# Kernel tuning notes

Hardware: AMD Instinct MI355X
Metric: run time of the kernel (lower is better)

Reference implementation:

```python
import jax, jax.numpy as jnp
import numpy as np

N = 100_000      # target ('paper') nodes
E_RAND = 500_000 # random metapath edges (self-loops added on top)
C = 256          # channels
H = 8            # heads
D = C // H       # proj_dim = 32
SEM = 128        # semantic attention hidden
NEG_SLOPE = 0.2


def _edges(k):
    e = jax.random.randint(k, (2, E_RAND), 0, N, dtype=jnp.int32)
    loops = jnp.broadcast_to(jnp.arange(N, dtype=jnp.int32), (2, N))
    return jnp.concatenate([e, loops], axis=1)  # [2, E_RAND + N]


def setup_inputs() -> dict:
    key = jax.random.key(0)
    ks = jax.random.split(key, 9)
    return {
        "x": jax.random.normal(ks[0], (N, C), dtype=jnp.float32),
        "W": jax.random.normal(ks[1], (D, C), dtype=jnp.float32) * (1.0 / np.sqrt(C)),
        "att1": jax.random.normal(ks[2], (H, 2 * D), dtype=jnp.float32) * (1.0 / np.sqrt(2 * D)),
        "att2": jax.random.normal(ks[3], (H, 2 * D), dtype=jnp.float32) * (1.0 / np.sqrt(2 * D)),
        "fc_w": jax.random.normal(ks[4], (SEM, C), dtype=jnp.float32) * (1.0 / np.sqrt(C)),
        "fc_b": jnp.zeros((SEM,), dtype=jnp.float32),
        "q": jax.random.normal(ks[5], (SEM,), dtype=jnp.float32) * (1.0 / np.sqrt(SEM)),
        "ei1": _edges(ks[6]),
        "ei2": _edges(ks[7]),
    }


def _segment_softmax(e, dst, num_nodes):
    # numerically stable softmax over edges grouped by destination node
    m = jax.ops.segment_max(e, dst, num_segments=num_nodes)      # [N, H]
    ex = jnp.exp(e - m[dst])                                     # [E, H]
    s = jax.ops.segment_sum(ex, dst, num_segments=num_nodes)     # [N, H]
    return ex / s[dst]


def _gat_layer(h, ei, att):
    # h: [N, d] projected target features; ei: [2, E]; att: [H, 2d]
    src, dst = ei[0], ei[1]
    n, d = h.shape
    a_dst, a_src = att[:, :d], att[:, d:]   # cat order in torch: [h_i(dst), h_j(src)]
    # per-edge attention logits [E, H] without materializing [E, H, 2d]
    e = jax.nn.leaky_relu(h[dst] @ a_dst.T + h[src] @ a_src.T, NEG_SLOPE)
    alpha = _segment_softmax(e, dst, n)                          # [E, H]
    m = h[src][:, None, :] * alpha[:, :, None]                   # [E, H, d]
    out = jax.ops.segment_sum(m, dst, num_segments=n)            # [N, H, d]
    return jax.nn.elu(out).reshape(n, H * d)                     # [N, H*d]


def reference(x, W, att1, att2, fc_w, fc_b, q, ei1, ei2):
    # type-specific projection (bias-free Linear): [N, C] -> [N, d]
    h = x @ W.T
    Z1 = _gat_layer(h, ei1, att1)
    Z2 = _gat_layer(h, ei2, att2)
    # semantic attention across meta-paths
    def score(Z):
        return (jnp.tanh(Z @ fc_w.T + fc_b) @ q).mean()
    V = jax.nn.softmax(jnp.stack([score(Z1), score(Z2)]))        # [2]
    return V[0] * Z1 + V[1] * Z2                                 # [N, C]
```

## Files before the change

kernel.cpp:

```cpp
#include <hip/hip_runtime.h>
#include <math.h>

#define Nn 100000
#define Cc 256
#define Dd 32
#define Hh 8
#define SEMk 128
#define PAD 32
#define NEG 0.2f

typedef __attribute__((ext_vector_type(8))) short bf16x8;
typedef __attribute__((ext_vector_type(4))) short s16x4;
typedef __attribute__((ext_vector_type(4))) float f32x4;

__device__ __forceinline__ short f2bf(float f) {
    unsigned u = __float_as_uint(f);
    u = (u + 0x7FFF + ((u >> 16) & 1)) >> 16;
    return (short)u;
}

__global__ __launch_bounds__(256) void k_wtrans(const float* __restrict__ W,
                                                float* __restrict__ Wt) {
    int i = blockIdx.x * 256 + threadIdx.x;
    if (i < Dd * Cc) {
        int j = i >> 5, k = i & 31;
        Wt[i] = W[k * Cc + j];
    }
}

__global__ __launch_bounds__(256) void k_fcwb(const float* __restrict__ fcw,
                                              short* __restrict__ fcwb) {
    int i = blockIdx.x * 256 + threadIdx.x;
    if (i < SEMk * Cc) fcwb[i] = f2bf(fcw[i]);
}

__global__ __launch_bounds__(256) void k_hproj(const float* __restrict__ x,
                                               const float* __restrict__ Wt,
                                               const float* __restrict__ att1,
                                               const float* __restrict__ att2,
                                               float* __restrict__ h,
                                               float* __restrict__ sd1, float* __restrict__ ss1,
                                               float* __restrict__ sd2, float* __restrict__ ss2) {
    __shared__ float4 xs[32 * 65];
    __shared__ float  wt[256 * 36];
    __shared__ float4 hs[32 * 9];
    __shared__ float  a1[8 * 68];
    __shared__ float  a2[8 * 68];

    int t = threadIdx.x;
    int nb = blockIdx.x * 32;

    const float4* xg = (const float4*)x + (size_t)nb * 64;
#pragma unroll
    for (int it = 0; it < 8; ++it) {
        int i = t + it * 256;
        xs[(i >> 6) * 65 + (i & 63)] = xg[i];
    }
    const float4* wg = (const float4*)Wt;
#pragma unroll
    for (int it = 0; it < 8; ++it) {
        int i = t + it * 256;
        *(float4*)&wt[(i >> 3) * 36 + (i & 7) * 4] = wg[i];
    }
#pragma unroll
    for (int it = 0; it < 2; ++it) {
        int i = t + it * 256;
        a1[(i >> 6) * 68 + (i & 63)] = att1[i];
        a2[(i >> 6) * 68 + (i & 63)] = att2[i];
    }
    __syncthreads();

    int nl = t >> 3;
    int dq = t & 7;
    float4 acc = make_float4(0.f, 0.f, 0.f, 0.f);
    const float4* xr = &xs[nl * 65];
#pragma unroll 4
    for (int j4 = 0; j4 < 64; ++j4) {
        float4 xv = xr[j4];
        float4 w0 = *(const float4*)&wt[(j4 * 4 + 0) * 36 + dq * 4];
        float4 w1 = *(const float4*)&wt[(j4 * 4 + 1) * 36 + dq * 4];
        float4 w2 = *(const float4*)&wt[(j4 * 4 + 2) * 36 + dq * 4];
        float4 w3 = *(const float4*)&wt[(j4 * 4 + 3) * 36 + dq * 4];
        acc.x += xv.x * w0.x + xv.y * w1.x + xv.z * w2.x + xv.w * w3.x;
        acc.y += xv.x * w0.y + xv.y * w1.y + xv.z * w2.y + xv.w * w3.y;
        acc.z += xv.x * w0.z + xv.y * w1.z + xv.z * w2.z + xv.w * w3.z;
        acc.w += xv.x * w0.w + xv.y * w1.w + xv.z * w2.w + xv.w * w3.w;
    }
    ((float4*)h)[(size_t)(nb + nl) * 8 + dq] = acc;
    hs[nl * 9 + dq] = acc;
    __syncthreads();

    int nl2 = t >> 3;
    int hh = t & 7;
    float d1 = 0.f, s1 = 0.f, d2 = 0.f, s2 = 0.f;
#pragma unroll
    for (int d4 = 0; d4 < 8; ++d4) {
        float4 hv = hs[nl2 * 9 + d4];
        float4 ad1 = *(const float4*)&a1[hh * 68 + d4 * 4];
        float4 as1 = *(const float4*)&a1[hh * 68 + 32 + d4 * 4];
        float4 ad2 = *(const float4*)&a2[hh * 68 + d4 * 4];
        float4 as2 = *(const float4*)&a2[hh * 68 + 32 + d4 * 4];
        d1 += hv.x * ad1.x + hv.y * ad1.y + hv.z * ad1.z + hv.w * ad1.w;
        s1 += hv.x * as1.x + hv.y * as1.y + hv.z * as1.z + hv.w * as1.w;
        d2 += hv.x * ad2.x + hv.y * ad2.y + hv.z * ad2.z + hv.w * ad2.w;
        s2 += hv.x * as2.x + hv.y * as2.y + hv.z * as2.z + hv.w * as2.w;
    }
    int n = nb + nl2;
    sd1[n * 8 + hh] = d1; ss1[n * 8 + hh] = s1;
    sd2[n * 8 + hh] = d2; ss2[n * 8 + hh] = s2;
}

__global__ __launch_bounds__(256) void k_scatter(const int* __restrict__ ei, int E,
                                                 int* __restrict__ cnt, int* __restrict__ slots) {
    int e = blockIdx.x * 256 + threadIdx.x;
    if (e >= E) return;
    int s = ei[e];
    int d = ei[E + e];
    int pos = atomicAdd(&cnt[d], 1);
    if (pos < PAD) slots[d * PAD + pos] = s;
}

__global__ __launch_bounds__(256) void k_gat(const float* __restrict__ h,
                                             const float* __restrict__ sdst,
                                             const float* __restrict__ ssrc,
                                             const int* __restrict__ cnt,
                                             const int* __restrict__ slots,
                                             float* __restrict__ Z) {
    int gid = blockIdx.x * 256 + threadIdx.x;
    int n = gid >> 6;
    int lane = gid & 63;
    if (n >= Nn) return;
    int deg = cnt[n]; if (deg > PAD) deg = PAD;
    int hh = lane >> 3;
    int sub = lane & 7;
    float sd = sdst[n * 8 + hh];
    int sval = slots[n * PAD + (lane & 31)];
    const float4* h4 = (const float4*)h;

    float ssum = 0.f;
    float4 acc = make_float4(0.f, 0.f, 0.f, 0.f);

    int cs0 = __shfl(sval, 0);
    int cs1 = __shfl(sval, 1);
    int cs2 = __shfl(sval, 2);
    int cs3 = __shfl(sval, 3);
    cs1 = (1 < deg) ? cs1 : n;
    cs2 = (2 < deg) ? cs2 : n;
    cs3 = (3 < deg) ? cs3 : n;
    float  ca0 = ssrc[(size_t)cs0 * 8 + hh];
    float  ca1 = ssrc[(size_t)cs1 * 8 + hh];
    float  ca2 = ssrc[(size_t)cs2 * 8 + hh];
    float  ca3 = ssrc[(size_t)cs3 * 8 + hh];
    float4 cv0 = h4[(size_t)cs0 * 8 + sub];
    float4 cv1 = h4[(size_t)cs1 * 8 + sub];
    float4 cv2 = h4[(size_t)cs2 * 8 + sub];
    float4 cv3 = h4[(size_t)cs3 * 8 + sub];

    int base = 0;
    for (;;) {
        int nb = base + 4;
        bool more = nb < deg;
        int ns0, ns1, ns2, ns3;
        float na0, na1, na2, na3;
        float4 nv0, nv1, nv2, nv3;
        if (more) {
            ns0 = __shfl(sval, nb + 0);
            ns1 = __shfl(sval, nb + 1);
            ns2 = __shfl(sval, nb + 2);
            ns3 = __shfl(sval, nb + 3);
            ns1 = (nb + 1 < deg) ? ns1 : n;
            ns2 = (nb + 2 < deg) ? ns2 : n;
            ns3 = (nb + 3 < deg) ? ns3 : n;
            na0 = ssrc[(size_t)ns0 * 8 + hh];
            na1 = ssrc[(size_t)ns1 * 8 + hh];
            na2 = ssrc[(size_t)ns2 * 8 + hh];
            na3 = ssrc[(size_t)ns3 * 8 + hh];
            nv0 = h4[(size_t)ns0 * 8 + sub];
            nv1 = h4[(size_t)ns1 * 8 + sub];
            nv2 = h4[(size_t)ns2 * 8 + sub];
            nv3 = h4[(size_t)ns3 * 8 + sub];
        }
        {
            float ev, w;
            ev = sd + ca0; ev = ev > 0.f ? ev : NEG * ev;
            w = __expf(ev);
            acc.x += w * cv0.x; acc.y += w * cv0.y; acc.z += w * cv0.z; acc.w += w * cv0.w;
            ssum += w;
            ev = sd + ca1; ev = ev > 0.f ? ev : NEG * ev;
            w = __expf(ev); w = (base + 1 < deg) ? w : 0.f;
            acc.x += w * cv1.x; acc.y += w * cv1.y; acc.z += w * cv1.z; acc.w += w * cv1.w;
            ssum += w;
            ev = sd + ca2; ev = ev > 0.f ? ev : NEG * ev;
            w = __expf(ev); w = (base + 2 < deg) ? w : 0.f;
            acc.x += w * cv2.x; acc.y += w * cv2.y; acc.z += w * cv2.z; acc.w += w * cv2.w;
            ssum += w;
            ev = sd + ca3; ev = ev > 0.f ? ev : NEG * ev;
            w = __expf(ev); w = (base + 3 < deg) ? w : 0.f;
            acc.x += w * cv3.x; acc.y += w * cv3.y; acc.z += w * cv3.z; acc.w += w * cv3.w;
            ssum += w;
        }
        if (!more) break;
        base = nb;
        cs0 = ns0; cs1 = ns1; cs2 = ns2; cs3 = ns3;
        ca0 = na0; ca1 = na1; ca2 = na2; ca3 = na3;
        cv0 = nv0; cv1 = nv1; cv2 = nv2; cv3 = nv3;
    }

    float inv = 1.f / ssum;
    float4 o;
    o.x = acc.x * inv; o.y = acc.y * inv; o.z = acc.z * inv; o.w = acc.w * inv;
    o.x = o.x > 0.f ? o.x : __expf(o.x) - 1.f;
    o.y = o.y > 0.f ? o.y : __expf(o.y) - 1.f;
    o.z = o.z > 0.f ? o.z : __expf(o.z) - 1.f;
    o.w = o.w > 0.f ? o.w : __expf(o.w) - 1.f;
    ((float4*)Z)[(size_t)n * 64 + lane] = o;
}

__device__ __forceinline__ float fast_tanh(float x) {
    return 1.f - 2.f / (1.f + __expf(2.f * x));
}

__global__ __launch_bounds__(256) void k_score(const float* __restrict__ Z,
                        const short* __restrict__ fcwb,
                        const float* __restrict__ fcb,
                        const float* __restrict__ q,
                        float* __restrict__ Sacc) {
    int t = threadIdx.x;
    int lane = t & 63;
    int wid = t >> 6;
    int nodebase = blockIdx.x * 64 + wid * 16;
    if (nodebase >= Nn) return;
    int col = lane & 15;
    int quad = lane >> 4;

    const float* zp = Z + (size_t)(nodebase + col) * Cc + quad * 8;
    bf16x8 af[8];
#pragma unroll
    for (int ks = 0; ks < 8; ++ks) {
        float4 f0 = *(const float4*)(zp + ks * 32);
        float4 f1 = *(const float4*)(zp + ks * 32 + 4);
        bf16x8 a;
        a[0] = f2bf(f0.x); a[1] = f2bf(f0.y); a[2] = f2bf(f0.z); a[3] = f2bf(f0.w);
        a[4] = f2bf(f1.x); a[5] = f2bf(f1.y); a[6] = f2bf(f1.z); a[7] = f2bf(f1.w);
        af[ks] = a;
    }

    f32x4 acc[8];
#pragma unroll
    for (int tt = 0; tt < 8; ++tt) { acc[tt][0] = 0.f; acc[tt][1] = 0.f; acc[tt][2] = 0.f; acc[tt][3] = 0.f; }

    const short* brow = fcwb + (size_t)col * Cc + quad * 8;
#pragma unroll
    for (int ks = 0; ks < 8; ++ks) {
#pragma unroll
        for (int tt = 0; tt < 8; ++tt) {
            bf16x8 b = *(const bf16x8*)(brow + tt * 4096 + ks * 32);
            acc[tt] = __builtin_amdgcn_mfma_f32_16x16x32_bf16(af[ks], b, acc[tt], 0, 0, 0);
        }
    }

    float local = 0.f;
#pragma unroll
    for (int tt = 0; tt < 8; ++tt) {
        int sem = tt * 16 + col;
        float b = fcb[sem], qq = q[sem];
#pragma unroll
        for (int r = 0; r < 4; ++r) local += fast_tanh(acc[tt][r] + b) * qq;
    }
#pragma unroll
    for (int off = 32; off > 0; off >>= 1) local += __shfl_down(local, off);
    if (lane == 0) atomicAdd(&Sacc[(blockIdx.x & 15) * 16], local);
}

__global__ __launch_bounds__(256) void k_combine(float* __restrict__ out,
                                                 const float* __restrict__ Z2,
                                                 const float* __restrict__ S) {
    float s1 = 0.f, s2 = 0.f;
#pragma unroll
    for (int i = 0; i < 16; ++i) { s1 += S[i * 16]; s2 += S[256 + i * 16]; }
    s1 *= (1.f / (float)Nn);
    s2 *= (1.f / (float)Nn);
    float mx = fmaxf(s1, s2);
    float e1 = __expf(s1 - mx), e2 = __expf(s2 - mx);
    float inv = 1.f / (e1 + e2);
    float V0 = e1 * inv, V1 = e2 * inv;
    size_t i = (size_t)blockIdx.x * 256 + threadIdx.x;
    if (i < (size_t)Nn * 64) {
        float4 a = ((float4*)out)[i];
        float4 b = ((const float4*)Z2)[i];
        a.x = V0 * a.x + V1 * b.x;
        a.y = V0 * a.y + V1 * b.y;
        a.z = V0 * a.z + V1 * b.z;
        a.w = V0 * a.w + V1 * b.w;
        ((float4*)out)[i] = a;
    }
}

extern "C" void kernel_launch(void* const* d_in, const int* in_sizes, int n_in,
                              void* d_out, int out_size, void* d_ws, size_t ws_size,
                              hipStream_t stream) {
    const float* x    = (const float*)d_in[0];
    const float* W    = (const float*)d_in[1];
    const float* att1 = (const float*)d_in[2];
    const float* att2 = (const float*)d_in[3];
    const float* fcw  = (const float*)d_in[4];
    const float* fcb  = (const float*)d_in[5];
    const float* q    = (const float*)d_in[6];
    const int*   ei1  = (const int*)d_in[7];
    const int*   ei2  = (const int*)d_in[8];
    int E1 = in_sizes[7] / 2;
    int E2 = in_sizes[8] / 2;
    float* out = (float*)d_out;

    char* ws = (char*)d_ws;
    size_t off = 0;
    auto alloc = [&](size_t bytes) -> char* {
        char* p = ws + off;
        off = (off + bytes + 255) & ~(size_t)255;
        return p;
    };
    float* Z2   = (float*)alloc((size_t)Nn * Cc * 4);
    float* h    = (float*)alloc((size_t)Nn * Dd * 4);
    float* sd1  = (float*)alloc((size_t)Nn * Hh * 4);
    float* ss1  = (float*)alloc((size_t)Nn * Hh * 4);
    float* sd2  = (float*)alloc((size_t)Nn * Hh * 4);
    float* ss2  = (float*)alloc((size_t)Nn * Hh * 4);
    int*   cnt  = (int*)alloc((size_t)2 * Nn * 4);
    float* red  = (float*)alloc(2048);
    float* Wt   = (float*)alloc((size_t)Dd * Cc * 4);
    short* fcwb = (short*)alloc((size_t)SEMk * Cc * 2);
    int*   slt1 = (int*)alloc((size_t)Nn * PAD * 4);
    int*   slt2 = (int*)alloc((size_t)Nn * PAD * 4);
    (void)ws_size; (void)n_in; (void)out_size;

    hipMemsetAsync(cnt, 0, (size_t)2 * Nn * 4, stream);
    hipMemsetAsync(red, 0, 2048, stream);

    k_wtrans<<<(Dd * Cc + 255) / 256, 256, 0, stream>>>(W, Wt);
    k_fcwb<<<(SEMk * Cc + 255) / 256, 256, 0, stream>>>(fcw, fcwb);
    k_hproj<<<Nn / 32, 256, 0, stream>>>(x, Wt, att1, att2, h, sd1, ss1, sd2, ss2);
    k_scatter<<<(E1 + 255) / 256, 256, 0, stream>>>(ei1, E1, cnt, slt1);
    k_scatter<<<(E2 + 255) / 256, 256, 0, stream>>>(ei2, E2, cnt + Nn, slt2);
    k_gat<<<(Nn * 64) / 256, 256, 0, stream>>>(h, sd1, ss1, cnt, slt1, out);
    k_gat<<<(Nn * 64) / 256, 256, 0, stream>>>(h, sd2, ss2, cnt + Nn, slt2, Z2);
    int nblk = (Nn + 63) / 64;
    k_score<<<nblk, 256, 0, stream>>>(out, fcwb, fcb, q, red);
    k_score<<<nblk, 256, 0, stream>>>(Z2, fcwb, fcb, q, red + 256);
    k_combine<<<(Nn * 64) / 256, 256, 0, stream>>>(out, Z2, red);
}
```

Measured before the change: 565.2 us.

## Merge paired launches, prescale logits for exp2, double-buffer GAT gathers

```diff
diff --git a/kernel.cpp b/kernel.cpp
--- a/kernel.cpp
+++ b/kernel.cpp
@@ -8,6 +8,15 @@
 #define SEMk 128
 #define PAD 32
 #define NEG 0.2f
+#define NB1 25000
+#define NBS 1563
+
+#if __has_builtin(__builtin_amdgcn_exp2f)
+#define EXP2(x) __builtin_amdgcn_exp2f(x)
+#else
+#define EXP2(x) exp2f(x)
+#endif
+#define LOG2E 1.44269504088896f
 
 typedef __attribute__((ext_vector_type(8))) short bf16x8;
 typedef __attribute__((ext_vector_type(4))) short s16x4;
@@ -19,18 +28,15 @@
     return (short)u;
 }
 
-__global__ __launch_bounds__(256) void k_wtrans(const float* __restrict__ W,
-                                                float* __restrict__ Wt) {
+__global__ __launch_bounds__(256) void k_prep(const float* __restrict__ W,
+                                              float* __restrict__ Wt,
+                                              const float* __restrict__ fcw,
+                                              short* __restrict__ fcwb) {
     int i = blockIdx.x * 256 + threadIdx.x;
     if (i < Dd * Cc) {
         int j = i >> 5, k = i & 31;
         Wt[i] = W[k * Cc + j];
     }
-}
-
-__global__ __launch_bounds__(256) void k_fcwb(const float* __restrict__ fcw,
-                                              short* __restrict__ fcwb) {
-    int i = blockIdx.x * 256 + threadIdx.x;
     if (i < SEMk * Cc) fcwb[i] = f2bf(fcw[i]);
 }
 
@@ -106,104 +112,97 @@
         s2 += hv.x * as2.x + hv.y * as2.y + hv.z * as2.z + hv.w * as2.w;
     }
     int n = nb + nl2;
-    sd1[n * 8 + hh] = d1; ss1[n * 8 + hh] = s1;
-    sd2[n * 8 + hh] = d2; ss2[n * 8 + hh] = s2;
-}
-
-__global__ __launch_bounds__(256) void k_scatter(const int* __restrict__ ei, int E,
-                                                 int* __restrict__ cnt, int* __restrict__ slots) {
-    int e = blockIdx.x * 256 + threadIdx.x;
-    if (e >= E) return;
+    sd1[n * 8 + hh] = d1 * LOG2E; ss1[n * 8 + hh] = s1 * LOG2E;
+    sd2[n * 8 + hh] = d2 * LOG2E; ss2[n * 8 + hh] = s2 * LOG2E;
+}
+
+__global__ __launch_bounds__(256) void k_scatter(const int* __restrict__ ei1, int E1,
+                                                 const int* __restrict__ ei2, int E2,
+                                                 int* __restrict__ cnt,
+                                                 int* __restrict__ slt1,
+                                                 int* __restrict__ slt2) {
+    int id = blockIdx.x * 256 + threadIdx.x;
+    const int* ei; int e, EE; int* c; int* sl;
+    if (id < E1) { ei = ei1; e = id; EE = E1; c = cnt; sl = slt1; }
+    else {
+        e = id - E1;
+        if (e >= E2) return;
+        ei = ei2; EE = E2; c = cnt + Nn; sl = slt2;
+    }
     int s = ei[e];
-    int d = ei[E + e];
-    int pos = atomicAdd(&cnt[d], 1);
-    if (pos < PAD) slots[d * PAD + pos] = s;
-}
-
-__global__ __launch_bounds__(256) void k_gat(const float* __restrict__ h,
-                                             const float* __restrict__ sdst,
-                                             const float* __restrict__ ssrc,
-                                             const int* __restrict__ cnt,
-                                             const int* __restrict__ slots,
-                                             float* __restrict__ Z) {
-    int gid = blockIdx.x * 256 + threadIdx.x;
-    int n = gid >> 6;
-    int lane = gid & 63;
-    if (n >= Nn) return;
-    int deg = cnt[n]; if (deg > PAD) deg = PAD;
+    int d = ei[EE + e];
+    int pos = atomicAdd(&c[d], 1);
+    if (pos < PAD) sl[d * PAD + pos] = s;
+}
+
+#define LOADC(S0,S1,S2,S3,A0,A1,A2,A3,V0,V1,V2,V3,BB) do {                         \
+    S0 = __shfl(sval, (BB) + 0); S1 = __shfl(sval, (BB) + 1);                      \
+    S2 = __shfl(sval, (BB) + 2); S3 = __shfl(sval, (BB) + 3);                      \
+    S1 = ((BB) + 1 < deg) ? S1 : n;                                                \
+    S2 = ((BB) + 2 < deg) ? S2 : n;                                                \
+    S3 = ((BB) + 3 < deg) ? S3 : n;                                                \
+    A0 = ssrc[(unsigned)S0 * 8u + hh]; A1 = ssrc[(unsigned)S1 * 8u + hh];          \
+    A2 = ssrc[(unsigned)S2 * 8u + hh]; A3 = ssrc[(unsigned)S3 * 8u + hh];          \
+    V0 = h4[(unsigned)S0 * 8u + sub];  V1 = h4[(unsigned)S1 * 8u + sub];           \
+    V2 = h4[(unsigned)S2 * 8u + sub];  V3 = h4[(unsigned)S3 * 8u + sub];           \
+} while (0)
+
+#define CONS(A0,A1,A2,A3,V0,V1,V2,V3,BB) do {                                      \
+    float ev_, w_;                                                                 \
+    ev_ = sd + A0; ev_ = ev_ > 0.f ? ev_ : NEG * ev_; w_ = EXP2(ev_);              \
+    acc.x += w_ * V0.x; acc.y += w_ * V0.y; acc.z += w_ * V0.z; acc.w += w_ * V0.w; ssum += w_; \
+    ev_ = sd + A1; ev_ = ev_ > 0.f ? ev_ : NEG * ev_; w_ = EXP2(ev_);              \
+    w_ = ((BB) + 1 < deg) ? w_ : 0.f;                                              \
+    acc.x += w_ * V1.x; acc.y += w_ * V1.y; acc.z += w_ * V1.z; acc.w += w_ * V1.w; ssum += w_; \
+    ev_ = sd + A2; ev_ = ev_ > 0.f ? ev_ : NEG * ev_; w_ = EXP2(ev_);              \
+    w_ = ((BB) + 2 < deg) ? w_ : 0.f;                                              \
+    acc.x += w_ * V2.x; acc.y += w_ * V2.y; acc.z += w_ * V2.z; acc.w += w_ * V2.w; ssum += w_; \
+    ev_ = sd + A3; ev_ = ev_ > 0.f ? ev_ : NEG * ev_; w_ = EXP2(ev_);              \
+    w_ = ((BB) + 3 < deg) ? w_ : 0.f;                                              \
+    acc.x += w_ * V3.x; acc.y += w_ * V3.y; acc.z += w_ * V3.z; acc.w += w_ * V3.w; ssum += w_; \
+} while (0)
+
+__global__ __launch_bounds__(256, 4) void k_gat(const float* __restrict__ h,
+                                                const float* __restrict__ sd1, const float* __restrict__ ss1,
+                                                const float* __restrict__ sd2, const float* __restrict__ ss2,
+                                                const int* __restrict__ cnt,
+                                                const int* __restrict__ slt1, const int* __restrict__ slt2,
+                                                float* __restrict__ Z1, float* __restrict__ Z2) {
+    int blk = blockIdx.x;
+    const float* sdst = sd1; const float* ssrc = ss1;
+    const int* cc = cnt; const int* sl = slt1; float* Z = Z1;
+    if (blk >= NB1) { blk -= NB1; sdst = sd2; ssrc = ss2; cc = cnt + Nn; sl = slt2; Z = Z2; }
+    int t = threadIdx.x;
+    int lane = t & 63;
+    int n = blk * 4 + (t >> 6);
+    int deg = cc[n]; if (deg > PAD) deg = PAD;
     int hh = lane >> 3;
     int sub = lane & 7;
     float sd = sdst[n * 8 + hh];
-    int sval = slots[n * PAD + (lane & 31)];
+    int sval = sl[n * PAD + (lane & 31)];
     const float4* h4 = (const float4*)h;
 
     float ssum = 0.f;
     float4 acc = make_float4(0.f, 0.f, 0.f, 0.f);
 
-    int cs0 = __shfl(sval, 0);
-    int cs1 = __shfl(sval, 1);
-    int cs2 = __shfl(sval, 2);
-    int cs3 = __shfl(sval, 3);
-    cs1 = (1 < deg) ? cs1 : n;
-    cs2 = (2 < deg) ? cs2 : n;
-    cs3 = (3 < deg) ? cs3 : n;
-    float  ca0 = ssrc[(size_t)cs0 * 8 + hh];
-    float  ca1 = ssrc[(size_t)cs1 * 8 + hh];
-    float  ca2 = ssrc[(size_t)cs2 * 8 + hh];
-    float  ca3 = ssrc[(size_t)cs3 * 8 + hh];
-    float4 cv0 = h4[(size_t)cs0 * 8 + sub];
-    float4 cv1 = h4[(size_t)cs1 * 8 + sub];
-    float4 cv2 = h4[(size_t)cs2 * 8 + sub];
-    float4 cv3 = h4[(size_t)cs3 * 8 + sub];
-
+    int as0, as1, as2, as3;  float aa0, aa1, aa2, aa3;  float4 av0, av1, av2, av3;
+    int bs0, bs1, bs2, bs3;  float ba0, ba1, ba2, ba3;  float4 bv0, bv1, bv2, bv3;
+
+    LOADC(as0, as1, as2, as3, aa0, aa1, aa2, aa3, av0, av1, av2, av3, 0);
     int base = 0;
     for (;;) {
-        int nb = base + 4;
-        bool more = nb < deg;
-        int ns0, ns1, ns2, ns3;
-        float na0, na1, na2, na3;
-        float4 nv0, nv1, nv2, nv3;
-        if (more) {
-            ns0 = __shfl(sval, nb + 0);
-            ns1 = __shfl(sval, nb + 1);
-            ns2 = __shfl(sval, nb + 2);
-            ns3 = __shfl(sval, nb + 3);
-            ns1 = (nb + 1 < deg) ? ns1 : n;
-            ns2 = (nb + 2 < deg) ? ns2 : n;
-            ns3 = (nb + 3 < deg) ? ns3 : n;
-            na0 = ssrc[(size_t)ns0 * 8 + hh];
-            na1 = ssrc[(size_t)ns1 * 8 + hh];
-            na2 = ssrc[(size_t)ns2 * 8 + hh];
-            na3 = ssrc[(size_t)ns3 * 8 + hh];
-            nv0 = h4[(size_t)ns0 * 8 + sub];
-            nv1 = h4[(size_t)ns1 * 8 + sub];
-            nv2 = h4[(size_t)ns2 * 8 + sub];
-            nv3 = h4[(size_t)ns3 * 8 + sub];
-        }
-        {
-            float ev, w;
-            ev = sd + ca0; ev = ev > 0.f ? ev : NEG * ev;
-            w = __expf(ev);
-            acc.x += w * cv0.x; acc.y += w * cv0.y; acc.z += w * cv0.z; acc.w += w * cv0.w;
-            ssum += w;
-            ev = sd + ca1; ev = ev > 0.f ? ev : NEG * ev;
-            w = __expf(ev); w = (base + 1 < deg) ? w : 0.f;
-            acc.x += w * cv1.x; acc.y += w * cv1.y; acc.z += w * cv1.z; acc.w += w * cv1.w;
-            ssum += w;
-            ev = sd + ca2; ev = ev > 0.f ? ev : NEG * ev;
-            w = __expf(ev); w = (base + 2 < deg) ? w : 0.f;
-            acc.x += w * cv2.x; acc.y += w * cv2.y; acc.z += w * cv2.z; acc.w += w * cv2.w;
-            ssum += w;
-            ev = sd + ca3; ev = ev > 0.f ? ev : NEG * ev;
-            w = __expf(ev); w = (base + 3 < deg) ? w : 0.f;
-            acc.x += w * cv3.x; acc.y += w * cv3.y; acc.z += w * cv3.z; acc.w += w * cv3.w;
-            ssum += w;
-        }
+        int nxt = base + 4;
+        bool more = nxt < deg;
+        if (more) LOADC(bs0, bs1, bs2, bs3, ba0, ba1, ba2, ba3, bv0, bv1, bv2, bv3, nxt);
+        CONS(aa0, aa1, aa2, aa3, av0, av1, av2, av3, base);
         if (!more) break;
-        base = nb;
-        cs0 = ns0; cs1 = ns1; cs2 = ns2; cs3 = ns3;
-        ca0 = na0; ca1 = na1; ca2 = na2; ca3 = na3;
-        cv0 = nv0; cv1 = nv1; cv2 = nv2; cv3 = nv3;
+        base = nxt;
+        nxt = base + 4;
+        more = nxt < deg;
+        if (more) LOADC(as0, as1, as2, as3, aa0, aa1, aa2, aa3, av0, av1, av2, av3, nxt);
+        CONS(ba0, ba1, ba2, ba3, bv0, bv1, bv2, bv3, base);
+        if (!more) break;
+        base = nxt;
     }
 
     float inv = 1.f / ssum;
@@ -220,15 +219,19 @@
     return 1.f - 2.f / (1.f + __expf(2.f * x));
 }
 
-__global__ __launch_bounds__(256) void k_score(const float* __restrict__ Z,
+__global__ __launch_bounds__(256) void k_score(const float* __restrict__ Z1,
+                        const float* __restrict__ Z2,
                         const short* __restrict__ fcwb,
                         const float* __restrict__ fcb,
                         const float* __restrict__ q,
                         float* __restrict__ Sacc) {
+    int blk = blockIdx.x;
+    const float* Z = Z1; float* bins = Sacc;
+    if (blk >= NBS) { blk -= NBS; Z = Z2; bins = Sacc + 256; }
     int t = threadIdx.x;
     int lane = t & 63;
     int wid = t >> 6;
-    int nodebase = blockIdx.x * 64 + wid * 16;
+    int nodebase = blk * 64 + wid * 16;
     if (nodebase >= Nn) return;
     int col = lane & 15;
     int quad = lane >> 4;
@@ -269,7 +272,7 @@
     }
 #pragma unroll
     for (int off = 32; off > 0; off >>= 1) local += __shfl_down(local, off);
-    if (lane == 0) atomicAdd(&Sacc[(blockIdx.x & 15) * 16], local);
+    if (lane == 0) atomicAdd(&bins[(blk & 15) * 16], local);
 }
 
 __global__ __launch_bounds__(256) void k_combine(float* __restrict__ out,
@@ -336,15 +339,10 @@
     hipMemsetAsync(cnt, 0, (size_t)2 * Nn * 4, stream);
     hipMemsetAsync(red, 0, 2048, stream);
 
-    k_wtrans<<<(Dd * Cc + 255) / 256, 256, 0, stream>>>(W, Wt);
-    k_fcwb<<<(SEMk * Cc + 255) / 256, 256, 0, stream>>>(fcw, fcwb);
+    k_prep<<<(SEMk * Cc + 255) / 256, 256, 0, stream>>>(W, Wt, fcw, fcwb);
     k_hproj<<<Nn / 32, 256, 0, stream>>>(x, Wt, att1, att2, h, sd1, ss1, sd2, ss2);
-    k_scatter<<<(E1 + 255) / 256, 256, 0, stream>>>(ei1, E1, cnt, slt1);
-    k_scatter<<<(E2 + 255) / 256, 256, 0, stream>>>(ei2, E2, cnt + Nn, slt2);
-    k_gat<<<(Nn * 64) / 256, 256, 0, stream>>>(h, sd1, ss1, cnt, slt1, out);
-    k_gat<<<(Nn * 64) / 256, 256, 0, stream>>>(h, sd2, ss2, cnt + Nn, slt2, Z2);
-    int nblk = (Nn + 63) / 64;
-    k_score<<<nblk, 256, 0, stream>>>(out, fcwb, fcb, q, red);
-    k_score<<<nblk, 256, 0, stream>>>(Z2, fcwb, fcb, q, red + 256);
+    k_scatter<<<(E1 + E2 + 255) / 256, 256, 0, stream>>>(ei1, E1, ei2, E2, cnt, slt1, slt2);
+    k_gat<<<2 * NB1, 256, 0, stream>>>(h, sd1, ss1, sd2, ss2, cnt, slt1, slt2, out, Z2);
+    k_score<<<2 * NBS, 256, 0, stream>>>(out, Z2, fcwb, fcb, q, red);
     k_combine<<<(Nn * 64) / 256, 256, 0, stream>>>(out, Z2, red);
 }
```

New measurement: 543.4 us. 1.04x faster.
